# Kernel tuning notes

Hardware: AMD Instinct MI355X
Metric: run time of the kernel (lower is better)

The kernel has to match this reference:

```python
import jax, jax.numpy as jnp
import numpy as np

B, S, D = 1, 2048, 2048
HQ, HKV = 32, 8
HD = D // HQ            # 64
G = HQ // HKV           # 4 query heads per kv head


def setup_inputs() -> dict:
    key = jax.random.key(0)
    ks = jax.random.split(key, 5)
    x = jax.random.normal(ks[0], (B, S, D), jnp.float32)
    # RoPE tables (theta = 10000), shape [S, HD//2]
    inv_freq = 1.0 / (10000.0 ** (np.arange(0, HD, 2, dtype=np.float64) / HD))
    angles = np.outer(np.arange(S, dtype=np.float64), inv_freq)
    freqs_cos = jnp.asarray(np.cos(angles), jnp.float32)
    freqs_sin = jnp.asarray(np.sin(angles), jnp.float32)
    # additive causal mask [1,1,S,S]: 0 on/below diagonal, large negative above
    i = jnp.arange(S)
    causal_mask = jnp.where(i[None, :] <= i[:, None], 0.0, -1e9).astype(jnp.float32)[None, None]
    sc = 1.0 / np.sqrt(D)
    Wq = jax.random.normal(ks[1], (D, HQ * HD), jnp.float32) * sc
    Wk = jax.random.normal(ks[2], (D, HKV * HD), jnp.float32) * sc
    Wv = jax.random.normal(ks[3], (D, HKV * HD), jnp.float32) * sc
    Wo = jax.random.normal(ks[4], (D, D), jnp.float32) * sc
    return {"x": x, "freqs_cos": freqs_cos, "freqs_sin": freqs_sin,
            "causal_mask": causal_mask, "Wq": Wq, "Wk": Wk, "Wv": Wv, "Wo": Wo}


def _rope(t, cos, sin):
    # t: [B,S,H,HD]; complex multiply on interleaved (even, odd) pairs
    b, s, h, d = t.shape
    t2 = t.reshape(b, s, h, d // 2, 2)
    t0, t1 = t2[..., 0], t2[..., 1]
    c = cos[None, :, None, :]
    sn = sin[None, :, None, :]
    out = jnp.stack([t0 * c - t1 * sn, t0 * sn + t1 * c], axis=-1)
    return out.reshape(b, s, h, d)


def reference(x, freqs_cos, freqs_sin, causal_mask, Wq, Wk, Wv, Wo):
    b, s, _ = x.shape
    q = (x @ Wq).reshape(b, s, HQ, HD)
    k = (x @ Wk).reshape(b, s, HKV, HD)
    v = (x @ Wv).reshape(b, s, HKV, HD)
    q = _rope(q, freqs_cos, freqs_sin)
    k = _rope(k, freqs_cos, freqs_sin)
    # GQA without materializing repeat_kv: group query heads per kv head
    q = q.transpose(0, 2, 1, 3).reshape(b, HKV, G, s, HD)   # [b,kv,g,s,d]
    k = k.transpose(0, 2, 1, 3)                              # [b,kv,s,d]
    v = v.transpose(0, 2, 1, 3)                              # [b,kv,s,d]
    scores = jnp.einsum('bkgsd,bktd->bkgst', q, k) / jnp.sqrt(jnp.float32(HD))
    scores = scores + causal_mask[:, :, None]                # [1,1,1,S,S] broadcast
    probs = jax.nn.softmax(scores, axis=-1)
    out = jnp.einsum('bkgst,bktd->bkgsd', probs, v)          # [b,kv,g,s,d]
    out = out.transpose(0, 3, 1, 2, 4).reshape(b, s, D)      # merge heads in (kv,g) order
    return out @ Wo
```

## Files before the change

### kernel.cpp

```cpp
#include <hip/hip_runtime.h>

#define SEQ 2048
#define DMODEL 2048

typedef __attribute__((ext_vector_type(8))) _Float16 half8;
typedef __attribute__((ext_vector_type(4))) float f32x4;
typedef __attribute__((ext_vector_type(16))) float f32x16;

typedef const __attribute__((address_space(1))) void* gptr_t;
typedef __attribute__((address_space(3))) void* lptr_t;

static __device__ __forceinline__ void gload16(const void* g, void* l) {
  __builtin_amdgcn_global_load_lds((gptr_t)g, (lptr_t)l, 16, 0, 0);
}

static __device__ __forceinline__ unsigned short f2h(float f) {
  _Float16 h = (_Float16)f;
  union { _Float16 h; unsigned short u; } v; v.h = h;
  return v.u;
}

static __device__ __forceinline__ unsigned int pkh2(float a, float b) {
  union { __fp16 __attribute__((ext_vector_type(2))) h; unsigned int u; } v;
  v.h = __builtin_amdgcn_cvt_pkrtz(a, b);
  return v.u;
}

__global__ void k_cvt(const float* __restrict__ in, unsigned short* __restrict__ out, int n) {
  int i = (blockIdx.x * 256 + threadIdx.x) * 4;
  if (i >= n) return;
  float4 v = *(const float4*)(in + i);
  ushort4 o;
  o.x = f2h(v.x); o.y = f2h(v.y); o.z = f2h(v.z); o.w = f2h(v.w);
  *(ushort4*)(out + i) = o;
}

__global__ void k_tcvt(const float* __restrict__ in, unsigned short* __restrict__ out,
                       int K, int N, int ldin) {
  __shared__ float tile[32][33];
  int n0 = blockIdx.x * 32, k0 = blockIdx.y * 32;
  int tx = threadIdx.x, ty = threadIdx.y;
  #pragma unroll
  for (int j = ty; j < 32; j += 8)
    tile[j][tx] = in[(long)(k0 + j) * ldin + n0 + tx];
  __syncthreads();
  #pragma unroll
  for (int j = ty; j < 32; j += 8)
    out[(long)(n0 + j) * K + k0 + tx] = f2h(tile[tx][j]);
}

__global__ void k_tvp(const unsigned short* __restrict__ in, unsigned short* __restrict__ out) {
  __shared__ unsigned short tile[32][33];
  int c0 = blockIdx.x * 32, s0 = blockIdx.y * 32;
  int tx = threadIdx.x, ty = threadIdx.y;
  #pragma unroll
  for (int j = ty; j < 32; j += 8)
    tile[j][tx] = in[(long)(s0 + j) * 512 + c0 + tx];
  __syncthreads();
  #pragma unroll
  for (int j = ty; j < 32; j += 8) {
    int c = c0 + j;
    int s = s0 + tx;
    int sp = (s & ~12) | ((s & 8) >> 1) | ((s & 4) << 1);
    out[((long)(c >> 6) * 64 + (c & 63)) * SEQ + sp] = tile[tx][j];
  }
}

template <int NF>
static __device__ __forceinline__ bool gemm_core(const unsigned short* __restrict__ A,
                                                 const unsigned short* __restrict__ B,
                                                 int K, char* SM, long m0, long n0,
                                                 int& wmO, int& wnO, f32x4 acc[4][NF]) {
  constexpr int BN = NF * 32;
  int t = threadIdx.x;
  int l = t & 63, w = t >> 6;
  int ks = w & 1, wm = (w >> 2) & 1, wn = (w >> 1) & 1;
  int lr = l & 15, lh = l >> 4;
  wmO = wm; wnO = wn;
  unsigned short* As = (unsigned short*)SM;
  unsigned short* Bs = (unsigned short*)(SM + 32768);

  const unsigned short* Ag = A + (m0 + (t >> 3)) * K + (((t & 7) ^ ((t >> 3) & 7)) * 8);
  const unsigned short* Bg = B + (n0 + (t >> 3)) * K + (((t & 7) ^ ((t >> 3) & 7)) * 8);

  #pragma unroll
  for (int i = 0; i < 4; i++)
    #pragma unroll
    for (int j = 0; j < NF; j++)
      acc[i][j] = (f32x4){0.f, 0.f, 0.f, 0.f};

#define STG(buf, k0) do { \
    gload16(Ag + (k0), As + (buf) * 8192 + t * 8); \
    gload16(Ag + 64 * K + (k0), As + (buf) * 8192 + 4096 + t * 8); \
    gload16(Bg + (k0), Bs + (buf) * (BN * 64) + t * 8); \
    if (t < (BN - 64) * 8) gload16(Bg + 64 * K + (k0), Bs + (buf) * (BN * 64) + 4096 + t * 8); \
  } while (0)

  int T = K >> 6;
  STG(0, 0);
  asm volatile("s_waitcnt vmcnt(0)" ::: "memory");
  __builtin_amdgcn_s_barrier();

  for (int ph = 0; ph < T; ph++) {
    if (ph + 1 < T) STG((ph + 1) & 1, (ph + 1) * 64);
    const unsigned short* Ab = As + (ph & 1) * 8192;
    const unsigned short* Bb = Bs + (ph & 1) * (BN * 64);
    half8 a[4], b[NF];
    #pragma unroll
    for (int mf = 0; mf < 4; mf++) {
      int ra = wm * 64 + mf * 16 + lr;
      a[mf] = *(const half8*)&Ab[ra * 64 + (((ks * 4 + lh) ^ (ra & 7)) * 8)];
    }
    #pragma unroll
    for (int nf = 0; nf < NF; nf++) {
      int rb = wn * (NF * 16) + nf * 16 + lr;
      b[nf] = *(const half8*)&Bb[rb * 64 + (((ks * 4 + lh) ^ (rb & 7)) * 8)];
    }
    #pragma unroll
    for (int mf = 0; mf < 4; mf++)
      #pragma unroll
      for (int nf = 0; nf < NF; nf++)
        acc[mf][nf] = __builtin_amdgcn_mfma_f32_16x16x32_f16(a[mf], b[nf], acc[mf][nf], 0, 0, 0);
    asm volatile("s_waitcnt vmcnt(0)" ::: "memory");
    __builtin_amdgcn_s_barrier();
  }
#undef STG

  __syncthreads();
  float* red = (float*)SM;
  int p = wm * 2 + wn;
  if (ks == 1) {
    #pragma unroll
    for (int mf = 0; mf < 4; mf++)
      #pragma unroll
      for (int nf = 0; nf < NF; nf++)
        *(f32x4*)&red[p * 4096 + l * 64 + (((mf * 4 + nf) ^ (l & 15)) << 2)] = acc[mf][nf];
  }
  __syncthreads();
  if (ks == 0) {
    #pragma unroll
    for (int mf = 0; mf < 4; mf++)
      #pragma unroll
      for (int nf = 0; nf < NF; nf++)
        acc[mf][nf] += *(const f32x4*)&red[p * 4096 + l * 64 + (((mf * 4 + nf) ^ (l & 15)) << 2)];
  }
  return ks == 0;
}

__global__ __launch_bounds__(512) void k_gemm(const unsigned short* __restrict__ A,
                                              const unsigned short* __restrict__ B,
                                              float* __restrict__ C, int M, int N, int K) {
  __shared__ __align__(16) char SM[65536];
  int l = threadIdx.x & 63;
  int lr = l & 15, lh = l >> 4;
  int bid = blockIdx.y * 16 + blockIdx.x;
  int swz = (bid & 7) * 32 + (bid >> 3);
  long m0 = (long)(swz >> 4) * 128, n0 = (long)(swz & 15) * 128;
  f32x4 acc[4][4];
  int wm, wn;
  bool own = gemm_core<4>(A, B, K, SM, m0, n0, wm, wn, acc);
  if (own) {
    #pragma unroll
    for (int mf = 0; mf < 4; mf++)
      #pragma unroll
      for (int nf = 0; nf < 4; nf++)
        #pragma unroll
        for (int i = 0; i < 4; i++)
          C[(m0 + wm * 64 + mf * 16 + lh * 4 + i) * N + n0 + wn * 64 + nf * 16 + lr] = acc[mf][nf][i];
  }
}

__global__ __launch_bounds__(512) void k_gemm_qkv(const unsigned short* __restrict__ A,
                                                  const unsigned short* __restrict__ B,
                                                  unsigned short* __restrict__ Qr,
                                                  unsigned short* __restrict__ Kr,
                                                  unsigned short* __restrict__ Vr,
                                                  const float* __restrict__ fc,
                                                  const float* __restrict__ fs, int K) {
  __shared__ __align__(16) char SM[65536];
  int l = threadIdx.x & 63;
  int lr = l & 15, lh = l >> 4;
  int bid = blockIdx.y * 32 + blockIdx.x;
  int swz = (bid & 7) * 64 + (bid >> 3);
  long m0 = (long)(swz >> 5) * 128, n0 = (long)(swz & 31) * 96;
  f32x4 acc[4][3];
  int wm, wn;
  bool own = gemm_core<3>(A, B, K, SM, m0, n0, wm, wn, acc);
  if (!own) return;

  const float SC = 0.125f * 1.44269504f;
  int n0i = (int)n0;
  #pragma unroll
  for (int mf = 0; mf < 4; mf++)
    #pragma unroll
    for (int i = 0; i < 4; i++) {
      int row = (int)m0 + wm * 64 + mf * 16 + lh * 4 + i;
      const float* fcr = fc + row * 32;
      const float* fsr = fs + row * 32;
      #pragma unroll
      for (int nf = 0; nf < 3; nf++) {
        float v = acc[mf][nf][i];
        int col = n0i + wn * 48 + nf * 16 + lr;
        if (col < 2560) {
          float pv = __shfl_xor(v, 1);
          float scl = col < 2048 ? SC : 1.0f;
          int j = (col & 63) >> 1;
          float c_ = fcr[j] * scl, s_ = fsr[j] * scl;
          float o = (lr & 1) ? (pv * s_ + v * c_) : (v * c_ - pv * s_);
          if (col < 2048) {
            Qr[(long)row * 2048 + col] = f2h(o);
          } else {
            int cc = col - 2048;
            Kr[((long)(cc >> 6) * SEQ + row) * 64 + (cc & 63)] = f2h(o);
          }
        } else {
          Vr[(long)row * 512 + (col - 2560)] = f2h(v);
        }
      }
    }
}

template <bool DG>
static __device__ __forceinline__ void attn_tile(const unsigned short* __restrict__ Ks,
                                                 const unsigned short* __restrict__ Vs,
                                                 int q, int hs, const half8 (&Qf)[4],
                                                 f32x16& O0, f32x16& O1, f32x4& lsum4) {
  half8 Kf[4], Vf[2][2];
  #pragma unroll
  for (int d = 0; d < 4; d++) {
    int e0 = d * 16 + 8 * hs;
    Kf[d] = *(const half8*)&Ks[q * 64 + (e0 ^ ((q & 7) << 3))];
  }
  #pragma unroll
  for (int ks = 0; ks < 2; ks++)
    #pragma unroll
    for (int nf = 0; nf < 2; nf++)
      Vf[ks][nf] = *(const half8*)&Vs[(2 * ks + hs) * 512 + (q + 32 * nf) * 8];

  f32x16 S;
  #pragma unroll
  for (int r = 0; r < 16; r++) S[r] = 0.f;
  #pragma unroll
  for (int d = 0; d < 4; d++)
    S = __builtin_amdgcn_mfma_f32_32x32x16_f16(Kf[d], Qf[d], S, 0, 0, 0);

  float p[16];
  #pragma unroll
  for (int r = 0; r < 16; r++) {
    float v = S[r];
    if (DG) {
      int key = (r & 3) + 8 * (r >> 2) + 4 * hs;
      if (key > q) v = -1e30f;
    }
    p[r] = __builtin_exp2f(v - 8.0f);
    lsum4[r & 3] += p[r];
  }

  union { unsigned int u[4]; half8 hh; } f0, f1;
  #pragma unroll
  for (int c = 0; c < 4; c++) {
    f0.u[c] = pkh2(p[2 * c], p[2 * c + 1]);
    f1.u[c] = pkh2(p[8 + 2 * c], p[9 + 2 * c]);
  }

  O0 = __builtin_amdgcn_mfma_f32_32x32x16_f16(f0.hh, Vf[0][0], O0, 0, 0, 0);
  O0 = __builtin_amdgcn_mfma_f32_32x32x16_f16(f1.hh, Vf[1][0], O0, 0, 0, 0);
  O1 = __builtin_amdgcn_mfma_f32_32x32x16_f16(f0.hh, Vf[0][1], O1, 0, 0, 0);
  O1 = __builtin_amdgcn_mfma_f32_32x32x16_f16(f1.hh, Vf[1][1], O1, 0, 0, 0);
}

__global__ __launch_bounds__(256) void k_attn(const unsigned short* __restrict__ Qr,
                                              const unsigned short* __restrict__ Kr,
                                              const unsigned short* __restrict__ Vg,
                                              unsigned short* __restrict__ Op,
                                              float* __restrict__ Lp) {
  __shared__ unsigned short KT[2][8192];
  __shared__ unsigned short VT[2][8192];

  int tt = threadIdx.x;
  int wid = tt >> 6, l = tt & 63;
  int q = l & 31, hs = l >> 5;
  int h = blockIdx.x, hkv = h >> 2;
  int y = blockIdx.y;
  int by = 15 - (y >> 1), z = y & 1;
  int h8 = (by + 2) >> 1;
  int sb = z ? h8 : 0, se = z ? by + 1 : h8;
  int dt = 4 * by + wid;
  int q0 = by * 128 + wid * 32;

  const unsigned short* Kh = Kr + (long)hkv * SEQ * 64;
  const unsigned short* Vh = Vg + (long)hkv * 64 * SEQ;

  int skr = tt >> 3, skc = tt & 7;
  const unsigned short* Ksrc = Kh + (long)skr * 64 + ((skc * 8) ^ ((skr & 7) << 3));
  const unsigned short* Vsrc = Vh + (long)(tt & 63) * SEQ + ((tt >> 6) * 8);

#define ASTAGE(si) do { \
    int buf_ = (si) & 1; \
    _Pragma("unroll") for (int sub_ = 0; sub_ < 4; sub_++) { \
      int t0_ = ((si) * 4 + sub_) * 32; \
      gload16(Ksrc + (long)t0_ * 64, &KT[buf_][sub_ * 2048 + tt * 8]); \
      gload16(Vsrc + t0_, &VT[buf_][sub_ * 2048 + tt * 8]); \
    } \
  } while (0)

  half8 Qf[4];
  #pragma unroll
  for (int d = 0; d < 4; d++)
    Qf[d] = *(const half8*)&Qr[(long)(q0 + q) * 2048 + h * 64 + d * 16 + 8 * hs];

  f32x16 O0, O1;
  #pragma unroll
  for (int r = 0; r < 16; r++) { O0[r] = 0.f; O1[r] = 0.f; }
  f32x4 lsum4 = (f32x4){0.f, 0.f, 0.f, 0.f};

  if (sb < se) {
    ASTAGE(sb);
    asm volatile("s_waitcnt vmcnt(0)" ::: "memory");
    __builtin_amdgcn_s_barrier();

    for (int si = sb; si < se; si++) {
      if (si + 1 < se) ASTAGE(si + 1);

      int buf = si & 1;
      const unsigned short* Kb = &KT[buf][0];
      const unsigned short* Vb = &VT[buf][0];
      int rem = dt - si * 4 + 1;
      if (rem > 4) {
        attn_tile<false>(Kb, Vb, q, hs, Qf, O0, O1, lsum4);
        attn_tile<false>(Kb + 2048, Vb + 2048, q, hs, Qf, O0, O1, lsum4);
        attn_tile<false>(Kb + 4096, Vb + 4096, q, hs, Qf, O0, O1, lsum4);
        attn_tile<false>(Kb + 6144, Vb + 6144, q, hs, Qf, O0, O1, lsum4);
      } else if (rem > 0) {
        for (int sub = 0; sub < rem - 1; sub++)
          attn_tile<false>(Kb + sub * 2048, Vb + sub * 2048, q, hs, Qf, O0, O1, lsum4);
        attn_tile<true>(Kb + (rem - 1) * 2048, Vb + (rem - 1) * 2048, q, hs, Qf, O0, O1, lsum4);
      }

      asm volatile("s_waitcnt vmcnt(0)" ::: "memory");
      __builtin_amdgcn_s_barrier();
    }
  }
#undef ASTAGE

  float ls = lsum4[0] + lsum4[1] + lsum4[2] + lsum4[3];
  ls += __shfl_xor(ls, 32);
  if (l < 32) Lp[z * 65536 + h * 2048 + q0 + l] = ls;
  unsigned short* Oz = Op + (long)z * 2048 * 2048;
  #pragma unroll
  for (int r = 0; r < 16; r++) {
    int row = (r & 3) + 8 * (r >> 2) + 4 * hs;
    Oz[(long)(q0 + row) * 2048 + h * 64 + q] = f2h(O0[r]);
    Oz[(long)(q0 + row) * 2048 + h * 64 + q + 32] = f2h(O1[r]);
  }
}

__global__ void k_merge(const unsigned short* __restrict__ Op, const float* __restrict__ Lp,
                        unsigned short* __restrict__ AO) {
  int row = blockIdx.x, t = threadIdx.x;
  int col = t * 8, h = col >> 6;
  float li = 1.f / (Lp[h * 2048 + row] + Lp[65536 + h * 2048 + row]);
  half8 a = *(const half8*)&Op[(long)row * 2048 + col];
  half8 b = *(const half8*)&Op[4194304l + (long)row * 2048 + col];
  half8 o;
  #pragma unroll
  for (int j = 0; j < 8; j++)
    o[j] = (_Float16)(((float)a[j] + (float)b[j]) * li);
  *(half8*)&AO[(long)row * 2048 + col] = o;
}

extern "C" void kernel_launch(void* const* d_in, const int* in_sizes, int n_in,
                              void* d_out, int out_size, void* d_ws, size_t ws_size,
                              hipStream_t stream) {
  const float* x  = (const float*)d_in[0];
  const float* fc = (const float*)d_in[1];
  const float* fs = (const float*)d_in[2];
  const float* Wq = (const float*)d_in[4];
  const float* Wk = (const float*)d_in[5];
  const float* Wv = (const float*)d_in[6];
  const float* Wo = (const float*)d_in[7];
  float* out = (float*)d_out;

  char* ws = (char*)d_ws;
  unsigned short* xb  = (unsigned short*)(ws);
  unsigned short* WT  = (unsigned short*)(ws + (8l  << 20));
  unsigned short* WoT = (unsigned short*)(ws + (20l << 20));
  unsigned short* Qr  = (unsigned short*)(ws + (28l << 20));
  unsigned short* Kr  = (unsigned short*)(ws + (36l << 20));
  unsigned short* Vr  = (unsigned short*)(ws + (38l << 20));
  unsigned short* Vt  = (unsigned short*)(ws + (40l << 20));
  unsigned short* Opp = (unsigned short*)(ws + (44l << 20));
  float*          Lp  = (float*)(ws + (60l << 20));
  unsigned short* AO  = xb;

  dim3 tb(32, 8);
  k_cvt<<<4096, 256, 0, stream>>>(x, xb, 2048 * 2048);
  k_tcvt<<<dim3(64, 64), tb, 0, stream>>>(Wq, WT, 2048, 2048, 2048);
  k_tcvt<<<dim3(16, 64), tb, 0, stream>>>(Wk, WT + 2048l * 2048, 2048, 512, 512);
  k_tcvt<<<dim3(16, 64), tb, 0, stream>>>(Wv, WT + 2560l * 2048, 2048, 512, 512);
  k_tcvt<<<dim3(64, 64), tb, 0, stream>>>(Wo, WoT, 2048, 2048, 2048);

  k_gemm_qkv<<<dim3(32, 16), 512, 0, stream>>>(xb, WT, Qr, Kr, Vr, fc, fs, 2048);

  k_tvp<<<dim3(16, 64), tb, 0, stream>>>(Vr, Vt);

  k_attn<<<dim3(32, 32), 256, 0, stream>>>(Qr, Kr, Vt, Opp, Lp);
  k_merge<<<2048, 256, 0, stream>>>(Opp, Lp, AO);

  k_gemm<<<dim3(16, 16), 512, 0, stream>>>(AO, WoT, out, 2048, 2048, 2048);
}
```

Before: 149.1 us.

## Fuse x fp32→fp16 conversion into QKV GEMM and split-KV merge into output GEMM

The QKV GEMM now loads fp32 x through registers, converts it to fp16 and writes it into swizzled LDS, which removes the separate k_cvt pass. The output GEMM reads both split-KV partial outputs and their row sums, then merges and normalizes them inside its A-tile staging, which removes k_merge and the AO buffer. Two launches and their global round trips go away. The cost is register-staged A loads in place of async global_load_lds, more global bytes per GEMM tile since fp32 x and two partials are reloaded by each column block, and the merge now accumulates in fp16 instead of fp32.

```diff
diff --git a/kernel.cpp b/kernel.cpp
--- a/kernel.cpp
+++ b/kernel.cpp
@@ -24,15 +24,6 @@
   union { __fp16 __attribute__((ext_vector_type(2))) h; unsigned int u; } v;
   v.h = __builtin_amdgcn_cvt_pkrtz(a, b);
   return v.u;
-}
-
-__global__ void k_cvt(const float* __restrict__ in, unsigned short* __restrict__ out, int n) {
-  int i = (blockIdx.x * 256 + threadIdx.x) * 4;
-  if (i >= n) return;
-  float4 v = *(const float4*)(in + i);
-  ushort4 o;
-  o.x = f2h(v.x); o.y = f2h(v.y); o.z = f2h(v.z); o.w = f2h(v.w);
-  *(ushort4*)(out + i) = o;
 }
 
 __global__ void k_tcvt(const float* __restrict__ in, unsigned short* __restrict__ out,
@@ -66,127 +57,112 @@
   }
 }
 
-template <int NF>
-static __device__ __forceinline__ bool gemm_core(const unsigned short* __restrict__ A,
-                                                 const unsigned short* __restrict__ B,
-                                                 int K, char* SM, long m0, long n0,
-                                                 int& wmO, int& wnO, f32x4 acc[4][NF]) {
-  constexpr int BN = NF * 32;
-  int t = threadIdx.x;
-  int l = t & 63, w = t >> 6;
-  int ks = w & 1, wm = (w >> 2) & 1, wn = (w >> 1) & 1;
-  int lr = l & 15, lh = l >> 4;
-  wmO = wm; wnO = wn;
-  unsigned short* As = (unsigned short*)SM;
-  unsigned short* Bs = (unsigned short*)(SM + 32768);
-
-  const unsigned short* Ag = A + (m0 + (t >> 3)) * K + (((t & 7) ^ ((t >> 3) & 7)) * 8);
-  const unsigned short* Bg = B + (n0 + (t >> 3)) * K + (((t & 7) ^ ((t >> 3) & 7)) * 8);
-
-  #pragma unroll
-  for (int i = 0; i < 4; i++)
-    #pragma unroll
-    for (int j = 0; j < NF; j++)
-      acc[i][j] = (f32x4){0.f, 0.f, 0.f, 0.f};
-
-#define STG(buf, k0) do { \
-    gload16(Ag + (k0), As + (buf) * 8192 + t * 8); \
-    gload16(Ag + 64 * K + (k0), As + (buf) * 8192 + 4096 + t * 8); \
-    gload16(Bg + (k0), Bs + (buf) * (BN * 64) + t * 8); \
-    if (t < (BN - 64) * 8) gload16(Bg + 64 * K + (k0), Bs + (buf) * (BN * 64) + 4096 + t * 8); \
-  } while (0)
-
-  int T = K >> 6;
-  STG(0, 0);
-  asm volatile("s_waitcnt vmcnt(0)" ::: "memory");
-  __builtin_amdgcn_s_barrier();
-
-  for (int ph = 0; ph < T; ph++) {
-    if (ph + 1 < T) STG((ph + 1) & 1, (ph + 1) * 64);
-    const unsigned short* Ab = As + (ph & 1) * 8192;
-    const unsigned short* Bb = Bs + (ph & 1) * (BN * 64);
-    half8 a[4], b[NF];
-    #pragma unroll
-    for (int mf = 0; mf < 4; mf++) {
-      int ra = wm * 64 + mf * 16 + lr;
-      a[mf] = *(const half8*)&Ab[ra * 64 + (((ks * 4 + lh) ^ (ra & 7)) * 8)];
-    }
-    #pragma unroll
-    for (int nf = 0; nf < NF; nf++) {
-      int rb = wn * (NF * 16) + nf * 16 + lr;
-      b[nf] = *(const half8*)&Bb[rb * 64 + (((ks * 4 + lh) ^ (rb & 7)) * 8)];
-    }
-    #pragma unroll
-    for (int mf = 0; mf < 4; mf++)
-      #pragma unroll
-      for (int nf = 0; nf < NF; nf++)
-        acc[mf][nf] = __builtin_amdgcn_mfma_f32_16x16x32_f16(a[mf], b[nf], acc[mf][nf], 0, 0, 0);
-    asm volatile("s_waitcnt vmcnt(0)" ::: "memory");
-    __builtin_amdgcn_s_barrier();
-  }
-#undef STG
-
-  __syncthreads();
-  float* red = (float*)SM;
-  int p = wm * 2 + wn;
-  if (ks == 1) {
-    #pragma unroll
-    for (int mf = 0; mf < 4; mf++)
-      #pragma unroll
-      for (int nf = 0; nf < NF; nf++)
-        *(f32x4*)&red[p * 4096 + l * 64 + (((mf * 4 + nf) ^ (l & 15)) << 2)] = acc[mf][nf];
-  }
-  __syncthreads();
-  if (ks == 0) {
-    #pragma unroll
-    for (int mf = 0; mf < 4; mf++)
-      #pragma unroll
-      for (int nf = 0; nf < NF; nf++)
-        acc[mf][nf] += *(const f32x4*)&red[p * 4096 + l * 64 + (((mf * 4 + nf) ^ (l & 15)) << 2)];
-  }
-  return ks == 0;
-}
-
-__global__ __launch_bounds__(512) void k_gemm(const unsigned short* __restrict__ A,
-                                              const unsigned short* __restrict__ B,
-                                              float* __restrict__ C, int M, int N, int K) {
-  __shared__ __align__(16) char SM[65536];
-  int l = threadIdx.x & 63;
-  int lr = l & 15, lh = l >> 4;
-  int bid = blockIdx.y * 16 + blockIdx.x;
-  int swz = (bid & 7) * 32 + (bid >> 3);
-  long m0 = (long)(swz >> 4) * 128, n0 = (long)(swz & 15) * 128;
-  f32x4 acc[4][4];
-  int wm, wn;
-  bool own = gemm_core<4>(A, B, K, SM, m0, n0, wm, wn, acc);
-  if (own) {
-    #pragma unroll
-    for (int mf = 0; mf < 4; mf++)
-      #pragma unroll
-      for (int nf = 0; nf < 4; nf++)
-        #pragma unroll
-        for (int i = 0; i < 4; i++)
-          C[(m0 + wm * 64 + mf * 16 + lh * 4 + i) * N + n0 + wn * 64 + nf * 16 + lr] = acc[mf][nf][i];
-  }
-}
-
-__global__ __launch_bounds__(512) void k_gemm_qkv(const unsigned short* __restrict__ A,
+__global__ __launch_bounds__(512) void k_gemm_qkv(const float* __restrict__ x,
                                                   const unsigned short* __restrict__ B,
                                                   unsigned short* __restrict__ Qr,
                                                   unsigned short* __restrict__ Kr,
                                                   unsigned short* __restrict__ Vr,
                                                   const float* __restrict__ fc,
-                                                  const float* __restrict__ fs, int K) {
+                                                  const float* __restrict__ fs) {
+  constexpr int NF = 3, BN = 96;
+  const int K = 2048, T = 32;
   __shared__ __align__(16) char SM[65536];
-  int l = threadIdx.x & 63;
+  unsigned short* As = (unsigned short*)SM;
+  unsigned short* Bs = (unsigned short*)(SM + 32768);
+
+  int t = threadIdx.x;
+  int l = t & 63, w = t >> 6;
+  int ks = w & 1, wm = (w >> 2) & 1, wn = (w >> 1) & 1;
   int lr = l & 15, lh = l >> 4;
   int bid = blockIdx.y * 32 + blockIdx.x;
   int swz = (bid & 7) * 64 + (bid >> 3);
   long m0 = (long)(swz >> 5) * 128, n0 = (long)(swz & 31) * 96;
-  f32x4 acc[4][3];
-  int wm, wn;
-  bool own = gemm_core<3>(A, B, K, SM, m0, n0, wm, wn, acc);
-  if (!own) return;
+
+  int r0 = t >> 3, c = t & 7;
+  int sw8 = (c ^ (r0 & 7)) * 8;
+  const float* xr = x + (m0 + r0) * 2048 + c * 8;
+  const unsigned short* Bg = B + (n0 + (t >> 3)) * K + (((t & 7) ^ ((t >> 3) & 7)) * 8);
+
+  float4 ar[4];
+#define ALOAD(ph) do { \
+    const float* p_ = xr + (ph) * 64; \
+    ar[0] = *(const float4*)p_; ar[1] = *(const float4*)(p_ + 4); \
+    ar[2] = *(const float4*)(p_ + 64 * 2048); ar[3] = *(const float4*)(p_ + 64 * 2048 + 4); \
+  } while (0)
+#define AWRITE(buf) do { \
+    union { _Float16 h[8]; uint4 u; } v0_, v1_; \
+    v0_.h[0]=(_Float16)ar[0].x; v0_.h[1]=(_Float16)ar[0].y; v0_.h[2]=(_Float16)ar[0].z; v0_.h[3]=(_Float16)ar[0].w; \
+    v0_.h[4]=(_Float16)ar[1].x; v0_.h[5]=(_Float16)ar[1].y; v0_.h[6]=(_Float16)ar[1].z; v0_.h[7]=(_Float16)ar[1].w; \
+    v1_.h[0]=(_Float16)ar[2].x; v1_.h[1]=(_Float16)ar[2].y; v1_.h[2]=(_Float16)ar[2].z; v1_.h[3]=(_Float16)ar[2].w; \
+    v1_.h[4]=(_Float16)ar[3].x; v1_.h[5]=(_Float16)ar[3].y; v1_.h[6]=(_Float16)ar[3].z; v1_.h[7]=(_Float16)ar[3].w; \
+    *(uint4*)&As[(buf) * 8192 + r0 * 64 + sw8] = v0_.u; \
+    *(uint4*)&As[(buf) * 8192 + (r0 + 64) * 64 + sw8] = v1_.u; \
+  } while (0)
+#define BSTG(buf, k0) do { \
+    gload16(Bg + (k0), Bs + (buf) * 6144 + t * 8); \
+    if (t < 256) gload16(Bg + 64 * K + (k0), Bs + (buf) * 6144 + 4096 + t * 8); \
+  } while (0)
+
+  f32x4 acc[4][NF];
+  #pragma unroll
+  for (int i = 0; i < 4; i++)
+    #pragma unroll
+    for (int j = 0; j < NF; j++)
+      acc[i][j] = (f32x4){0.f, 0.f, 0.f, 0.f};
+
+  ALOAD(0);
+  BSTG(0, 0);
+  asm volatile("s_waitcnt vmcnt(0)" ::: "memory");
+  AWRITE(0);
+  asm volatile("s_waitcnt lgkmcnt(0)" ::: "memory");
+  __builtin_amdgcn_s_barrier();
+
+  for (int ph = 0; ph < T; ph++) {
+    if (ph + 1 < T) { ALOAD(ph + 1); BSTG((ph + 1) & 1, (ph + 1) * 64); }
+    const unsigned short* Ab = As + (ph & 1) * 8192;
+    const unsigned short* Bb = Bs + (ph & 1) * 6144;
+    half8 a[4], b[NF];
+    #pragma unroll
+    for (int mf = 0; mf < 4; mf++) {
+      int ra = wm * 64 + mf * 16 + lr;
+      a[mf] = *(const half8*)&Ab[ra * 64 + (((ks * 4 + lh) ^ (ra & 7)) * 8)];
+    }
+    #pragma unroll
+    for (int nf = 0; nf < NF; nf++) {
+      int rb = wn * (NF * 16) + nf * 16 + lr;
+      b[nf] = *(const half8*)&Bb[rb * 64 + (((ks * 4 + lh) ^ (rb & 7)) * 8)];
+    }
+    #pragma unroll
+    for (int mf = 0; mf < 4; mf++)
+      #pragma unroll
+      for (int nf = 0; nf < NF; nf++)
+        acc[mf][nf] = __builtin_amdgcn_mfma_f32_16x16x32_f16(a[mf], b[nf], acc[mf][nf], 0, 0, 0);
+    asm volatile("s_waitcnt vmcnt(0)" ::: "memory");
+    if (ph + 1 < T) AWRITE((ph + 1) & 1);
+    asm volatile("s_waitcnt lgkmcnt(0)" ::: "memory");
+    __builtin_amdgcn_s_barrier();
+  }
+#undef ALOAD
+#undef AWRITE
+#undef BSTG
+
+  __syncthreads();
+  float* red = (float*)SM;
+  int p = wm * 2 + wn;
+  if (ks == 1) {
+    #pragma unroll
+    for (int mf = 0; mf < 4; mf++)
+      #pragma unroll
+      for (int nf = 0; nf < NF; nf++)
+        *(f32x4*)&red[p * 4096 + l * 64 + (((mf * 4 + nf) ^ (l & 15)) << 2)] = acc[mf][nf];
+  }
+  __syncthreads();
+  if (ks == 1) return;
+  #pragma unroll
+  for (int mf = 0; mf < 4; mf++)
+    #pragma unroll
+    for (int nf = 0; nf < NF; nf++)
+      acc[mf][nf] += *(const f32x4*)&red[p * 4096 + l * 64 + (((mf * 4 + nf) ^ (l & 15)) << 2)];
 
   const float SC = 0.125f * 1.44269504f;
   int n0i = (int)n0;
@@ -198,7 +174,7 @@
       const float* fcr = fc + row * 32;
       const float* fsr = fs + row * 32;
       #pragma unroll
-      for (int nf = 0; nf < 3; nf++) {
+      for (int nf = 0; nf < NF; nf++) {
         float v = acc[mf][nf][i];
         int col = n0i + wn * 48 + nf * 16 + lr;
         if (col < 2560) {
@@ -220,6 +196,126 @@
     }
 }
 
+__global__ __launch_bounds__(512) void k_gemm_out(const unsigned short* __restrict__ Op,
+                                                  const float* __restrict__ Lp,
+                                                  const unsigned short* __restrict__ B,
+                                                  float* __restrict__ C) {
+  constexpr int NF = 4;
+  const int K = 2048, N = 2048, T = 32;
+  __shared__ __align__(16) char SM[65536];
+  unsigned short* As = (unsigned short*)SM;
+  unsigned short* Bs = (unsigned short*)(SM + 32768);
+
+  int t = threadIdx.x;
+  int l = t & 63, w = t >> 6;
+  int ks = w & 1, wm = (w >> 2) & 1, wn = (w >> 1) & 1;
+  int lr = l & 15, lh = l >> 4;
+  int bid = blockIdx.y * 16 + blockIdx.x;
+  int swz = (bid & 7) * 32 + (bid >> 3);
+  long m0 = (long)(swz >> 4) * 128, n0 = (long)(swz & 15) * 128;
+
+  int r0 = t >> 3, c = t & 7;
+  int sw8 = (c ^ (r0 & 7)) * 8;
+  long s0 = m0 + r0, s1 = m0 + r0 + 64;
+  const unsigned short* Oa = Op + s0 * 2048 + c * 8;
+  const unsigned short* Ob = Op + 4194304l + s0 * 2048 + c * 8;
+  const unsigned short* Bg = B + (n0 + (t >> 3)) * K + (((t & 7) ^ ((t >> 3) & 7)) * 8);
+
+  half8 p00, p01, p10, p11;
+  float li0, li1;
+#define ALOAD(ph) do { \
+    p00 = *(const half8*)(Oa + (ph) * 64); \
+    p01 = *(const half8*)(Ob + (ph) * 64); \
+    p10 = *(const half8*)(Oa + 64 * 2048 + (ph) * 64); \
+    p11 = *(const half8*)(Ob + 64 * 2048 + (ph) * 64); \
+    li0 = 1.f / (Lp[(ph) * 2048 + s0] + Lp[65536 + (ph) * 2048 + s0]); \
+    li1 = 1.f / (Lp[(ph) * 2048 + s1] + Lp[65536 + (ph) * 2048 + s1]); \
+  } while (0)
+#define AWRITE(buf) do { \
+    _Float16 l0_ = (_Float16)li0, l1_ = (_Float16)li1; \
+    half8 m0_, m1_; \
+    _Pragma("unroll") for (int j_ = 0; j_ < 8; j_++) { \
+      m0_[j_] = (p00[j_] + p01[j_]) * l0_; \
+      m1_[j_] = (p10[j_] + p11[j_]) * l1_; \
+    } \
+    *(half8*)&As[(buf) * 8192 + r0 * 64 + sw8] = m0_; \
+    *(half8*)&As[(buf) * 8192 + (r0 + 64) * 64 + sw8] = m1_; \
+  } while (0)
+#define BSTG(buf, k0) do { \
+    gload16(Bg + (k0), Bs + (buf) * 8192 + t * 8); \
+    gload16(Bg + 64 * K + (k0), Bs + (buf) * 8192 + 4096 + t * 8); \
+  } while (0)
+
+  f32x4 acc[4][NF];
+  #pragma unroll
+  for (int i = 0; i < 4; i++)
+    #pragma unroll
+    for (int j = 0; j < NF; j++)
+      acc[i][j] = (f32x4){0.f, 0.f, 0.f, 0.f};
+
+  ALOAD(0);
+  BSTG(0, 0);
+  asm volatile("s_waitcnt vmcnt(0)" ::: "memory");
+  AWRITE(0);
+  asm volatile("s_waitcnt lgkmcnt(0)" ::: "memory");
+  __builtin_amdgcn_s_barrier();
+
+  for (int ph = 0; ph < T; ph++) {
+    if (ph + 1 < T) { ALOAD(ph + 1); BSTG((ph + 1) & 1, (ph + 1) * 64); }
+    const unsigned short* Ab = As + (ph & 1) * 8192;
+    const unsigned short* Bb = Bs + (ph & 1) * 8192;
+    half8 a[4], b[NF];
+    #pragma unroll
+    for (int mf = 0; mf < 4; mf++) {
+      int ra = wm * 64 + mf * 16 + lr;
+      a[mf] = *(const half8*)&Ab[ra * 64 + (((ks * 4 + lh) ^ (ra & 7)) * 8)];
+    }
+    #pragma unroll
+    for (int nf = 0; nf < NF; nf++) {
+      int rb = wn * (NF * 16) + nf * 16 + lr;
+      b[nf] = *(const half8*)&Bb[rb * 64 + (((ks * 4 + lh) ^ (rb & 7)) * 8)];
+    }
+    #pragma unroll
+    for (int mf = 0; mf < 4; mf++)
+      #pragma unroll
+      for (int nf = 0; nf < NF; nf++)
+        acc[mf][nf] = __builtin_amdgcn_mfma_f32_16x16x32_f16(a[mf], b[nf], acc[mf][nf], 0, 0, 0);
+    asm volatile("s_waitcnt vmcnt(0)" ::: "memory");
+    if (ph + 1 < T) AWRITE((ph + 1) & 1);
+    asm volatile("s_waitcnt lgkmcnt(0)" ::: "memory");
+    __builtin_amdgcn_s_barrier();
+  }
+#undef ALOAD
+#undef AWRITE
+#undef BSTG
+
+  __syncthreads();
+  float* red = (float*)SM;
+  int p = wm * 2 + wn;
+  if (ks == 1) {
+    #pragma unroll
+    for (int mf = 0; mf < 4; mf++)
+      #pragma unroll
+      for (int nf = 0; nf < NF; nf++)
+        *(f32x4*)&red[p * 4096 + l * 64 + (((mf * 4 + nf) ^ (l & 15)) << 2)] = acc[mf][nf];
+  }
+  __syncthreads();
+  if (ks == 1) return;
+  #pragma unroll
+  for (int mf = 0; mf < 4; mf++)
+    #pragma unroll
+    for (int nf = 0; nf < NF; nf++)
+      acc[mf][nf] += *(const f32x4*)&red[p * 4096 + l * 64 + (((mf * 4 + nf) ^ (l & 15)) << 2)];
+
+  #pragma unroll
+  for (int mf = 0; mf < 4; mf++)
+    #pragma unroll
+    for (int nf = 0; nf < NF; nf++)
+      #pragma unroll
+      for (int i = 0; i < 4; i++)
+        C[(m0 + wm * 64 + mf * 16 + lh * 4 + i) * N + n0 + wn * 64 + nf * 16 + lr] = acc[mf][nf][i];
+}
+
 template <bool DG>
 static __device__ __forceinline__ void attn_tile(const unsigned short* __restrict__ Ks,
                                                  const unsigned short* __restrict__ Vs,
@@ -355,20 +451,6 @@
   }
 }
 
-__global__ void k_merge(const unsigned short* __restrict__ Op, const float* __restrict__ Lp,
-                        unsigned short* __restrict__ AO) {
-  int row = blockIdx.x, t = threadIdx.x;
-  int col = t * 8, h = col >> 6;
-  float li = 1.f / (Lp[h * 2048 + row] + Lp[65536 + h * 2048 + row]);
-  half8 a = *(const half8*)&Op[(long)row * 2048 + col];
-  half8 b = *(const half8*)&Op[4194304l + (long)row * 2048 + col];
-  half8 o;
-  #pragma unroll
-  for (int j = 0; j < 8; j++)
-    o[j] = (_Float16)(((float)a[j] + (float)b[j]) * li);
-  *(half8*)&AO[(long)row * 2048 + col] = o;
-}
-
 extern "C" void kernel_launch(void* const* d_in, const int* in_sizes, int n_in,
                               void* d_out, int out_size, void* d_ws, size_t ws_size,
                               hipStream_t stream) {
@@ -382,30 +464,26 @@
   float* out = (float*)d_out;
 
   char* ws = (char*)d_ws;
-  unsigned short* xb  = (unsigned short*)(ws);
-  unsigned short* WT  = (unsigned short*)(ws + (8l  << 20));
-  unsigned short* WoT = (unsigned short*)(ws + (20l << 20));
-  unsigned short* Qr  = (unsigned short*)(ws + (28l << 20));
-  unsigned short* Kr  = (unsigned short*)(ws + (36l << 20));
-  unsigned short* Vr  = (unsigned short*)(ws + (38l << 20));
-  unsigned short* Vt  = (unsigned short*)(ws + (40l << 20));
-  unsigned short* Opp = (unsigned short*)(ws + (44l << 20));
-  float*          Lp  = (float*)(ws + (60l << 20));
-  unsigned short* AO  = xb;
+  unsigned short* WT  = (unsigned short*)(ws);
+  unsigned short* WoT = (unsigned short*)(ws + (12l << 20));
+  unsigned short* Qr  = (unsigned short*)(ws + (20l << 20));
+  unsigned short* Kr  = (unsigned short*)(ws + (28l << 20));
+  unsigned short* Vr  = (unsigned short*)(ws + (30l << 20));
+  unsigned short* Vt  = (unsigned short*)(ws + (32l << 20));
+  unsigned short* Opp = (unsigned short*)(ws + (34l << 20));
+  float*          Lp  = (float*)(ws + (50l << 20));
 
   dim3 tb(32, 8);
-  k_cvt<<<4096, 256, 0, stream>>>(x, xb, 2048 * 2048);
   k_tcvt<<<dim3(64, 64), tb, 0, stream>>>(Wq, WT, 2048, 2048, 2048);
   k_tcvt<<<dim3(16, 64), tb, 0, stream>>>(Wk, WT + 2048l * 2048, 2048, 512, 512);
   k_tcvt<<<dim3(16, 64), tb, 0, stream>>>(Wv, WT + 2560l * 2048, 2048, 512, 512);
   k_tcvt<<<dim3(64, 64), tb, 0, stream>>>(Wo, WoT, 2048, 2048, 2048);
 
-  k_gemm_qkv<<<dim3(32, 16), 512, 0, stream>>>(xb, WT, Qr, Kr, Vr, fc, fs, 2048);
+  k_gemm_qkv<<<dim3(32, 16), 512, 0, stream>>>(x, WT, Qr, Kr, Vr, fc, fs);
 
   k_tvp<<<dim3(16, 64), tb, 0, stream>>>(Vr, Vt);
 
   k_attn<<<dim3(32, 32), 256, 0, stream>>>(Qr, Kr, Vt, Opp, Lp);
-  k_merge<<<2048, 256, 0, stream>>>(Opp, Lp, AO);
-
-  k_gemm<<<dim3(16, 16), 512, 0, stream>>>(AO, WoT, out, 2048, 2048, 2048);
-}
+
+  k_gemm_out<<<dim3(16, 16), 512, 0, stream>>>(Opp, Lp, WoT, out);
+}
```

Result: slower. 168.0 us (+12.7%).
